# Kernel optimization log

Hardware: AMD Instinct MI355X
Metric: run time of the kernel (lower is better)

Reference implementation:

```python
import jax, jax.numpy as jnp
import numpy as np

IN_F, OUT_F, R = 4096, 4096, 16
SCALING = 32.0 / R  # lora_alpha / r


def setup_inputs() -> dict:
    key = jax.random.key(0)
    kx, kw, kb, ka, kB = jax.random.split(key, 5)
    bound_w = 1.0 / np.sqrt(IN_F)  # kaiming_uniform a=sqrt(5) on (out,in) -> U(-1/sqrt(in), 1/sqrt(in))
    x = jax.random.normal(kx, (4, 4096, IN_F), dtype=jnp.float32)
    weight = jax.random.uniform(kw, (OUT_F, IN_F), jnp.float32, -bound_w, bound_w)
    bias = jax.random.uniform(kb, (OUT_F,), jnp.float32, -bound_w, bound_w)
    lora_A = jax.random.uniform(ka, (R, IN_F), jnp.float32, -bound_w, bound_w)
    # B is zero-init in the module; use small random values so the LoRA path is exercised
    lora_B = jax.random.normal(kB, (OUT_F, R), dtype=jnp.float32) * 0.01
    return {"x": x, "weight": weight, "bias": bias, "lora_A": lora_A, "lora_B": lora_B}


def reference(x, weight, bias, lora_A, lora_B):
    # base: F.linear(x, W, b) = x @ W.T + b
    base_out = jnp.einsum("bsi,oi->bso", x, weight) + bias
    # low-rank path: (x @ A.T) @ B.T * scaling  (dropout=0 -> identity)
    xr = jnp.einsum("bsi,ri->bsr", x, lora_A)  # [b, s, r]
    lora_out = jnp.einsum("bsr,or->bso", xr, lora_B) * SCALING
    return base_out + lora_out
```

## Files before the change

kernel.cpp:

```cpp
#include <hip/hip_runtime.h>
#include <hip/hip_bf16.h>


typedef __attribute__((ext_vector_type(8))) short bf16x8;
typedef __attribute__((ext_vector_type(4))) float f32x4;
typedef __attribute__((ext_vector_type(4))) unsigned short u16x4;

#define M_DIM 16384
#define N_DIM 4096
#define K_DIM 4096
#define NT 64

__device__ __forceinline__ unsigned short f2bf(float f) {
    unsigned int u = __builtin_bit_cast(unsigned int, f);
    unsigned int r = u + 0x7FFFu + ((u >> 16) & 1u);
    return (unsigned short)(r >> 16);
}

__device__ __forceinline__ void async16(const void* g, void* l) {
    __builtin_amdgcn_global_load_lds(
        (const __attribute__((address_space(1))) unsigned int*)g,
        (__attribute__((address_space(3))) unsigned int*)l,
        16, 0, 0);
}

__global__ void __launch_bounds__(256) cast_x_kernel(
    const float4* __restrict__ x, u16x4* __restrict__ y, int n4) {
    int i = blockIdx.x * blockDim.x + threadIdx.x;
    int stride = gridDim.x * blockDim.x;
    for (; i < n4; i += stride) {
        float4 v = x[i];
        u16x4 o = { f2bf(v.x), f2bf(v.y), f2bf(v.z), f2bf(v.w) };
        y[i] = o;
    }
}

__global__ void __launch_bounds__(256) weff_kernel(
    const float* __restrict__ W, const float* __restrict__ lA,
    const float* __restrict__ lB, unsigned short* __restrict__ out) {
    constexpr int K = K_DIM, R = 16;
    constexpr float S = 2.0f;
    int o = blockIdx.x;
    int t = threadIdx.x;
    float b[R];
#pragma unroll
    for (int r = 0; r < R; ++r) b[r] = lB[o * R + r];
#pragma unroll
    for (int c = 0; c < 4; ++c) {
        int i = c * 1024 + t * 4;
        float4 wv = *reinterpret_cast<const float4*>(&W[o * K + i]);
        float sx = 0.f, sy = 0.f, sz = 0.f, sw = 0.f;
#pragma unroll
        for (int r = 0; r < R; ++r) {
            float4 a = *reinterpret_cast<const float4*>(&lA[r * K + i]);
            sx += b[r] * a.x; sy += b[r] * a.y;
            sz += b[r] * a.z; sw += b[r] * a.w;
        }
        u16x4 ov = { f2bf(wv.x + S * sx), f2bf(wv.y + S * sy),
                     f2bf(wv.z + S * sz), f2bf(wv.w + S * sw) };
        *reinterpret_cast<u16x4*>(&out[o * K + i]) = ov;
    }
}

#define STAGE(G, h, tt, bsel, moff)                                           \
    do {                                                                      \
        const unsigned short* g0 = (G) +                                      \
            (size_t)((h) * 128 + wid * 16 + rc) * K_DIM + (tt) * 64 + cc * 8; \
        char* l0 = lds + (bsel) * 65536 + (moff) + (h) * 16384 + wid * 2048;  \
        async16(g0, l0);                                                      \
        async16(g0 + 8 * K_DIM, l0 + 1024);                                   \
    } while (0)

#define LDA_TO(dst, mh, bsel)                                                 \
    _Pragma("unroll") for (int mm = 0; mm < 4; ++mm)                          \
    _Pragma("unroll") for (int ks = 0; ks < 2; ++ks)                          \
        dst[mm][ks] = *(const bf16x8*)(lds + (bsel) * 65536 +                 \
            ((aBase + ((mh) * 4 + mm) * 2048) ^ (ks << 6)));

#define LDB_TO(nh, bsel)                                                      \
    _Pragma("unroll") for (int nn = 0; nn < 2; ++nn)                          \
    _Pragma("unroll") for (int ks = 0; ks < 2; ++ks)                          \
        br[(nh) * 2 + nn][ks] = *(const bf16x8*)(lds + (bsel) * 65536 +       \
            ((bBase + ((nh) * 2 + nn) * 2048) ^ (ks << 6)));

#define MM_Q(src, mh, nh)                                                     \
    __builtin_amdgcn_s_setprio(1);                                            \
    _Pragma("unroll") for (int ks = 0; ks < 2; ++ks)                          \
    _Pragma("unroll") for (int mm = 0; mm < 4; ++mm)                          \
    _Pragma("unroll") for (int nn = 0; nn < 2; ++nn)                          \
        acc[(mh) * 4 + mm][(nh) * 2 + nn] =                                   \
            __builtin_amdgcn_mfma_f32_16x16x32_bf16(                          \
                src[mm][ks], br[(nh) * 2 + nn][ks],                           \
                acc[(mh) * 4 + mm][(nh) * 2 + nn], 0, 0, 0);                  \
    __builtin_amdgcn_s_setprio(0)

#define CFENCE() asm volatile("" ::: "memory")

__global__ void __launch_bounds__(512, 2) gemm2b_kernel(
    const unsigned short* __restrict__ A,
    const unsigned short* __restrict__ B,
    const float* __restrict__ bias,
    float* __restrict__ C) {
    __shared__ __align__(1024) char lds[131072];

    const int tid = threadIdx.x;
    const int lane = tid & 63, wid = tid >> 6;
    const int wm = wid >> 2, wn = wid & 3;
    const int lr = lane & 15, lg = lane >> 4;

    const int bid = blockIdx.x;
    const int swz = (bid & 7) * 128 + (bid >> 3);
    const int bm = swz >> 4, bn = swz & 15;

    const unsigned short* Ag = A + (size_t)bm * 256 * K_DIM;
    const unsigned short* Bg = B + (size_t)bn * 256 * K_DIM;

    const int lam = lane ^ (lane >> 3);
    const int rc = lam >> 3, cc = lam & 7;

    const int kx0 = (lg * 16) ^ ((lr & 7) << 4);
    const int aBase = (wm * 128 + lr) * 128 + kx0;
    const int bBase = 32768 + (wn * 64 + lr) * 128 + kx0;

    f32x4 acc[8][4] = {};
    bf16x8 arA[4][2], arB[4][2], br[4][2];

    STAGE(Bg, 0, 0, 0, 32768);
    STAGE(Bg, 1, 0, 0, 32768);
    STAGE(Ag, 0, 0, 0, 0);
    STAGE(Ag, 1, 0, 0, 0);
    STAGE(Bg, 0, 1, 1, 32768);
    STAGE(Bg, 1, 1, 1, 32768);
    asm volatile("s_waitcnt vmcnt(4)" ::: "memory");
    __builtin_amdgcn_s_barrier();
    CFENCE();

#pragma unroll 2
    for (int t = 0; t < NT; ++t) {
        const int bs = t & 1, bo = bs ^ 1;
        LDA_TO(arA, 0, bs);
        LDB_TO(0, bs);
        LDB_TO(1, bs);
        if (t + 1 < NT) {
            STAGE(Ag, 0, t + 1, bo, 0);
            STAGE(Ag, 1, t + 1, bo, 0);
        }
        MM_Q(arA, 0, 0);
        LDA_TO(arB, 1, bs);
        MM_Q(arA, 0, 1);
        CFENCE();
        __builtin_amdgcn_s_barrier();
        CFENCE();
        if (t + 2 < NT) STAGE(Bg, 0, t + 2, bs, 32768);
        MM_Q(arB, 1, 0);
        if (t + 2 < NT) STAGE(Bg, 1, t + 2, bs, 32768);
        MM_Q(arB, 1, 1);
        if (t < NT - 2) {
            asm volatile("s_waitcnt vmcnt(4)" ::: "memory");
        } else {
            asm volatile("s_waitcnt vmcnt(0)" ::: "memory");
        }
        __builtin_amdgcn_s_barrier();
        CFENCE();
    }

    const int row0 = bm * 256 + wm * 128;
    const int col0 = bn * 256 + wn * 64;
#pragma unroll
    for (int n = 0; n < 4; ++n) {
        const int col = col0 + n * 16 + lr;
        const float bv = bias[col];
#pragma unroll
        for (int m = 0; m < 8; ++m) {
            const int r0 = row0 + m * 16 + lg * 4;
#pragma unroll
            for (int r = 0; r < 4; ++r)
                C[(size_t)(r0 + r) * N_DIM + col] = acc[m][n][r] + bv;
        }
    }
}

extern "C" void kernel_launch(void* const* d_in, const int* in_sizes, int n_in,
                              void* d_out, int out_size, void* d_ws, size_t ws_size,
                              hipStream_t stream) {
    const float* x    = (const float*)d_in[0];
    const float* W    = (const float*)d_in[1];
    const float* bias = (const float*)d_in[2];
    const float* lA   = (const float*)d_in[3];
    const float* lB   = (const float*)d_in[4];
    float* out = (float*)d_out;

    unsigned short* xb   = (unsigned short*)d_ws;
    unsigned short* weff = (unsigned short*)((char*)d_ws + 134217728);

    cast_x_kernel<<<2048, 256, 0, stream>>>((const float4*)x, (u16x4*)xb,
                                            M_DIM * K_DIM / 4);
    weff_kernel<<<N_DIM, 256, 0, stream>>>(W, lA, lB, weff);
    gemm2b_kernel<<<(M_DIM / 256) * (N_DIM / 256), 512, 0, stream>>>(
        xb, weff, bias, out);
}
```

Baseline: 590.5 us.

## Pre-swizzle B into MFMA fragment layout and load it directly to registers

The weight-prep kernel now writes the effective bf16 weight in a fragment-major layout that matches the MFMA B operand lane order. The GEMM then reads B straight from global memory into registers, double-buffered across k-tiles, instead of staging it through LDS. Only A is still staged in LDS, which halves LDS use to 64KB and removes B's LDS writes, reads and the mid-iteration barrier. The cost is that B is now fetched per wave from global or L2 with no sharing through LDS across the waves in the wm dimension, and the register footprint grows.

```diff
diff --git a/kernel.cpp b/kernel.cpp
--- a/kernel.cpp
+++ b/kernel.cpp
@@ -58,15 +58,18 @@
         }
         u16x4 ov = { f2bf(wv.x + S * sx), f2bf(wv.y + S * sy),
                      f2bf(wv.z + S * sz), f2bf(wv.w + S * sw) };
-        *reinterpret_cast<u16x4*>(&out[o * K + i]) = ov;
+        const int frag = (o >> 4) * 128 + (i >> 5);
+        const int lane_ = (o & 15) + (((i >> 3) & 3) << 4);
+        const size_t addr = ((size_t)frag << 9) + (lane_ << 3) + (i & 7);
+        *reinterpret_cast<u16x4*>(&out[addr]) = ov;
     }
 }
 
-#define STAGE(G, h, tt, bsel, moff)                                           \
+#define STAGE(G, h, tt, bsel)                                                 \
     do {                                                                      \
         const unsigned short* g0 = (G) +                                      \
             (size_t)((h) * 128 + wid * 16 + rc) * K_DIM + (tt) * 64 + cc * 8; \
-        char* l0 = lds + (bsel) * 65536 + (moff) + (h) * 16384 + wid * 2048;  \
+        char* l0 = lds + (bsel) * 32768 + (h) * 16384 + wid * 2048;           \
         async16(g0, l0);                                                      \
         async16(g0 + 8 * K_DIM, l0 + 1024);                                   \
     } while (0)
@@ -74,34 +77,53 @@
 #define LDA_TO(dst, mh, bsel)                                                 \
     _Pragma("unroll") for (int mm = 0; mm < 4; ++mm)                          \
     _Pragma("unroll") for (int ks = 0; ks < 2; ++ks)                          \
-        dst[mm][ks] = *(const bf16x8*)(lds + (bsel) * 65536 +                 \
+        dst[mm][ks] = *(const bf16x8*)(lds + (bsel) * 32768 +                 \
             ((aBase + ((mh) * 4 + mm) * 2048) ^ (ks << 6)));
 
-#define LDB_TO(nh, bsel)                                                      \
-    _Pragma("unroll") for (int nn = 0; nn < 2; ++nn)                          \
+#define LOADB(dst, tt)                                                        \
+    _Pragma("unroll") for (int j = 0; j < 4; ++j)                             \
     _Pragma("unroll") for (int ks = 0; ks < 2; ++ks)                          \
-        br[(nh) * 2 + nn][ks] = *(const bf16x8*)(lds + (bsel) * 65536 +       \
-            ((bBase + ((nh) * 2 + nn) * 2048) ^ (ks << 6)));
+        dst[j][ks] = *(const bf16x8*)(Bt +                                    \
+            (((size_t)(bgrp + j) * 128 + (tt) * 2 + ks) << 9) + (lane << 3));
 
-#define MM_Q(src, mh, nh)                                                     \
+#define MMH(mh, BR)                                                           \
     __builtin_amdgcn_s_setprio(1);                                            \
     _Pragma("unroll") for (int ks = 0; ks < 2; ++ks)                          \
     _Pragma("unroll") for (int mm = 0; mm < 4; ++mm)                          \
-    _Pragma("unroll") for (int nn = 0; nn < 2; ++nn)                          \
-        acc[(mh) * 4 + mm][(nh) * 2 + nn] =                                   \
-            __builtin_amdgcn_mfma_f32_16x16x32_bf16(                          \
-                src[mm][ks], br[(nh) * 2 + nn][ks],                           \
-                acc[(mh) * 4 + mm][(nh) * 2 + nn], 0, 0, 0);                  \
+    _Pragma("unroll") for (int j = 0; j < 4; ++j)                             \
+        acc[(mh) * 4 + mm][j] = __builtin_amdgcn_mfma_f32_16x16x32_bf16(      \
+            ar[mm][ks], BR[j][ks], acc[(mh) * 4 + mm][j], 0, 0, 0);           \
     __builtin_amdgcn_s_setprio(0)
 
 #define CFENCE() asm volatile("" ::: "memory")
 
-__global__ void __launch_bounds__(512, 2) gemm2b_kernel(
+#define KTILE(t, BRCUR, BRNXT)                                                \
+    {                                                                         \
+        const int bs_ = (t) & 1, bo_ = bs_ ^ 1;                               \
+        if ((t) + 1 < NT) {                                                   \
+            STAGE(Ag, 0, (t) + 1, bo_);                                       \
+            STAGE(Ag, 1, (t) + 1, bo_);                                       \
+            CFENCE();   \
+            LOADB(BRNXT, (t) + 1);                                            \
+        }                                                                     \
+        CFENCE();                                                             \
+        LDA_TO(ar, 0, bs_);                                                   \
+        MMH(0, BRCUR);                                                        \
+        LDA_TO(ar, 1, bs_);                                                   \
+        MMH(1, BRCUR);                                                        \
+        if ((t) + 1 < NT) {                                                   \
+            asm volatile("s_waitcnt vmcnt(8)" ::: "memory");                  \
+            __builtin_amdgcn_s_barrier();                                     \
+            CFENCE();                                                         \
+        }                                                                     \
+    }
+
+__global__ void __launch_bounds__(512, 2) gemmbd_kernel(
     const unsigned short* __restrict__ A,
-    const unsigned short* __restrict__ B,
+    const unsigned short* __restrict__ Bt,
     const float* __restrict__ bias,
     float* __restrict__ C) {
-    __shared__ __align__(1024) char lds[131072];
+    __shared__ __align__(1024) char lds[65536];
 
     const int tid = threadIdx.x;
     const int lane = tid & 63, wid = tid >> 6;
@@ -113,55 +135,28 @@
     const int bm = swz >> 4, bn = swz & 15;
 
     const unsigned short* Ag = A + (size_t)bm * 256 * K_DIM;
-    const unsigned short* Bg = B + (size_t)bn * 256 * K_DIM;
+    const int bgrp = bn * 16 + wn * 4;
 
     const int lam = lane ^ (lane >> 3);
     const int rc = lam >> 3, cc = lam & 7;
 
     const int kx0 = (lg * 16) ^ ((lr & 7) << 4);
     const int aBase = (wm * 128 + lr) * 128 + kx0;
-    const int bBase = 32768 + (wn * 64 + lr) * 128 + kx0;
 
     f32x4 acc[8][4] = {};
-    bf16x8 arA[4][2], arB[4][2], br[4][2];
+    bf16x8 ar[4][2], brX[4][2], brY[4][2];
 
-    STAGE(Bg, 0, 0, 0, 32768);
-    STAGE(Bg, 1, 0, 0, 32768);
-    STAGE(Ag, 0, 0, 0, 0);
-    STAGE(Ag, 1, 0, 0, 0);
-    STAGE(Bg, 0, 1, 1, 32768);
-    STAGE(Bg, 1, 1, 1, 32768);
-    asm volatile("s_waitcnt vmcnt(4)" ::: "memory");
+    STAGE(Ag, 0, 0, 0);
+    STAGE(Ag, 1, 0, 0);
+    CFENCE();
+    LOADB(brX, 0);
+    asm volatile("s_waitcnt vmcnt(8)" ::: "memory");
     __builtin_amdgcn_s_barrier();
     CFENCE();
 
-#pragma unroll 2
-    for (int t = 0; t < NT; ++t) {
-        const int bs = t & 1, bo = bs ^ 1;
-        LDA_TO(arA, 0, bs);
-        LDB_TO(0, bs);
-        LDB_TO(1, bs);
-        if (t + 1 < NT) {
-            STAGE(Ag, 0, t + 1, bo, 0);
-            STAGE(Ag, 1, t + 1, bo, 0);
-        }
-        MM_Q(arA, 0, 0);
-        LDA_TO(arB, 1, bs);
-        MM_Q(arA, 0, 1);
-        CFENCE();
-        __builtin_amdgcn_s_barrier();
-        CFENCE();
-        if (t + 2 < NT) STAGE(Bg, 0, t + 2, bs, 32768);
-        MM_Q(arB, 1, 0);
-        if (t + 2 < NT) STAGE(Bg, 1, t + 2, bs, 32768);
-        MM_Q(arB, 1, 1);
-        if (t < NT - 2) {
-            asm volatile("s_waitcnt vmcnt(4)" ::: "memory");
-        } else {
-            asm volatile("s_waitcnt vmcnt(0)" ::: "memory");
-        }
-        __builtin_amdgcn_s_barrier();
-        CFENCE();
+    for (int tt = 0; tt < NT; tt += 2) {
+        KTILE(tt, brX, brY);
+        KTILE(tt + 1, brY, brX);
     }
 
     const int row0 = bm * 256 + wm * 128;
@@ -196,6 +191,6 @@
     cast_x_kernel<<<2048, 256, 0, stream>>>((const float4*)x, (u16x4*)xb,
                                             M_DIM * K_DIM / 4);
     weff_kernel<<<N_DIM, 256, 0, stream>>>(W, lA, lB, weff);
-    gemm2b_kernel<<<(M_DIM / 256) * (N_DIM / 256), 512, 0, stream>>>(
+    gemmbd_kernel<<<(M_DIM / 256) * (N_DIM / 256), 512, 0, stream>>>(
         xb, weff, bias, out);
 }
```

New measurement: 732.4 us. 24.0% more time.

## Simplify GEMM k-loop to single-barrier double buffering with one-tile prefetch

Applied to the files above, without the earlier changes.

Restructures the main GEMM loop so each k-tile issues all A and B global-to-LDS loads for the next tile at the start, computes the current tile, then drains with vmcnt(0) and one barrier. This replaces the previous schedule, which prefetched B two tiles ahead, split the compute with a mid-iteration barrier, and waited only partially. The aim is to cut barrier overhead and simplify the schedule, at the cost of less prefetch depth and a full memory drain every tile.

```diff
diff --git a/kernel.cpp b/kernel.cpp
--- a/kernel.cpp
+++ b/kernel.cpp
@@ -96,7 +96,29 @@
 
 #define CFENCE() asm volatile("" ::: "memory")
 
-__global__ void __launch_bounds__(512, 2) gemm2b_kernel(
+#define KTILE(t)                                                              \
+    {                                                                         \
+        const int bs_ = (t) & 1, bo_ = bs_ ^ 1;                               \
+        if ((t) + 1 < NT) {                                                   \
+            STAGE(Ag, 0, (t) + 1, bo_, 0);                                    \
+            STAGE(Ag, 1, (t) + 1, bo_, 0);                                    \
+            STAGE(Bg, 0, (t) + 1, bo_, 32768);                                \
+            STAGE(Bg, 1, (t) + 1, bo_, 32768);                                \
+        }                                                                     \
+        LDA_TO(arA, 0, bs_);                                                  \
+        LDB_TO(0, bs_);                                                       \
+        LDB_TO(1, bs_);                                                       \
+        MM_Q(arA, 0, 0);                                                      \
+        LDA_TO(arB, 1, bs_);                                                  \
+        MM_Q(arA, 0, 1);                                                      \
+        MM_Q(arB, 1, 0);                                                      \
+        MM_Q(arB, 1, 1);                                                      \
+        asm volatile("s_waitcnt vmcnt(0)" ::: "memory");                      \
+        __builtin_amdgcn_s_barrier();                                         \
+        CFENCE();                                                             \
+    }
+
+__global__ void __launch_bounds__(512, 2) gemm1b_kernel(
     const unsigned short* __restrict__ A,
     const unsigned short* __restrict__ B,
     const float* __restrict__ bias,
@@ -125,43 +147,17 @@
     f32x4 acc[8][4] = {};
     bf16x8 arA[4][2], arB[4][2], br[4][2];
 
+    STAGE(Ag, 0, 0, 0, 0);
+    STAGE(Ag, 1, 0, 0, 0);
     STAGE(Bg, 0, 0, 0, 32768);
     STAGE(Bg, 1, 0, 0, 32768);
-    STAGE(Ag, 0, 0, 0, 0);
-    STAGE(Ag, 1, 0, 0, 0);
-    STAGE(Bg, 0, 1, 1, 32768);
-    STAGE(Bg, 1, 1, 1, 32768);
-    asm volatile("s_waitcnt vmcnt(4)" ::: "memory");
+    asm volatile("s_waitcnt vmcnt(0)" ::: "memory");
     __builtin_amdgcn_s_barrier();
     CFENCE();
 
-#pragma unroll 2
-    for (int t = 0; t < NT; ++t) {
-        const int bs = t & 1, bo = bs ^ 1;
-        LDA_TO(arA, 0, bs);
-        LDB_TO(0, bs);
-        LDB_TO(1, bs);
-        if (t + 1 < NT) {
-            STAGE(Ag, 0, t + 1, bo, 0);
-            STAGE(Ag, 1, t + 1, bo, 0);
-        }
-        MM_Q(arA, 0, 0);
-        LDA_TO(arB, 1, bs);
-        MM_Q(arA, 0, 1);
-        CFENCE();
-        __builtin_amdgcn_s_barrier();
-        CFENCE();
-        if (t + 2 < NT) STAGE(Bg, 0, t + 2, bs, 32768);
-        MM_Q(arB, 1, 0);
-        if (t + 2 < NT) STAGE(Bg, 1, t + 2, bs, 32768);
-        MM_Q(arB, 1, 1);
-        if (t < NT - 2) {
-            asm volatile("s_waitcnt vmcnt(4)" ::: "memory");
-        } else {
-            asm volatile("s_waitcnt vmcnt(0)" ::: "memory");
-        }
-        __builtin_amdgcn_s_barrier();
-        CFENCE();
+    for (int tt = 0; tt < NT; tt += 2) {
+        KTILE(tt);
+        KTILE(tt + 1);
     }
 
     const int row0 = bm * 256 + wm * 128;
@@ -196,6 +192,6 @@
     cast_x_kernel<<<2048, 256, 0, stream>>>((const float4*)x, (u16x4*)xb,
                                             M_DIM * K_DIM / 4);
     weff_kernel<<<N_DIM, 256, 0, stream>>>(W, lA, lB, weff);
-    gemm2b_kernel<<<(M_DIM / 256) * (N_DIM / 256), 512, 0, stream>>>(
+    gemm1b_kernel<<<(M_DIM / 256) * (N_DIM / 256), 512, 0, stream>>>(
         xb, weff, bias, out);
 }
```

New measurement: 677.6 us. 1.15x slower.
